# Optimization experiments

Measured on AMD Instinct MI355X. Metric: run time of the kernel, lower is better.

Reference implementation:

```python
import jax, jax.numpy as jnp
import numpy as np

DIM = 1024
H = 16
DH = DIM // H
K = 4
B = 8
N = 2048
EPS = 1e-6


def _depthwise_conv_silu(x, w, n):
    # x: (B, N, C), w: (C, 1, K)  -- torch Conv1d depthwise, padding=K//2, truncate to n, SiLU
    pad = K // 2
    y = jax.lax.conv_general_dilated(
        x.transpose(0, 2, 1), w, window_strides=(1,), padding=[(pad, pad)],
        dimension_numbers=('NCH', 'OIH', 'NCH'), feature_group_count=x.shape[-1])
    y = y[..., :n]  # for even K the conv output is n+1; torch truncates
    return jax.nn.silu(y).transpose(0, 2, 1)


def _l2norm(x):
    return x / (jnp.linalg.norm(x, axis=-1, keepdims=True) + EPS)


def setup_inputs() -> dict:
    key = jax.random.key(0)
    ks = jax.random.split(key, 16)
    s = 1.0 / np.sqrt(DIM)
    d = dict(
        x=jax.random.normal(ks[0], (B, N, DIM), jnp.float32),
        Wq=jax.random.normal(ks[1], (DIM, DIM), jnp.float32) * s,
        bq=jnp.zeros((DIM,), jnp.float32),
        Wk=jax.random.normal(ks[2], (DIM, DIM), jnp.float32) * s,
        bk=jnp.zeros((DIM,), jnp.float32),
        Wv=jax.random.normal(ks[3], (DIM, DIM), jnp.float32) * s,
        bv=jnp.zeros((DIM,), jnp.float32),
        Wa=jax.random.normal(ks[4], (H, DIM), jnp.float32) * s,
        ba=jnp.zeros((H,), jnp.float32),
        Wb=jax.random.normal(ks[5], (H, DIM), jnp.float32) * s,
        bb=jnp.zeros((H,), jnp.float32),
        conv_q=jax.random.normal(ks[6], (DIM, 1, K), jnp.float32) * 0.5,
        conv_k=jax.random.normal(ks[7], (DIM, 1, K), jnp.float32) * 0.5,
        conv_v=jax.random.normal(ks[8], (DIM, 1, K), jnp.float32) * 0.5,
        Wo=jax.random.normal(ks[9], (DIM, DIM), jnp.float32) * s,
        bo=jnp.zeros((DIM,), jnp.float32),
    )
    return d


def _forward(x, Wq, bq, Wk, bk, Wv, bv, Wa, ba, Wb, bb, conv_q, conv_k, conv_v, Wo, bo):
    b_, n_, c_ = x.shape
    q = _l2norm(_depthwise_conv_silu(jax.nn.silu(x @ Wq.T + bq), conv_q, n_))
    k = _l2norm(_depthwise_conv_silu(jax.nn.silu(x @ Wk.T + bk), conv_k, n_))
    v = _depthwise_conv_silu(jax.nn.silu(x @ Wv.T + bv), conv_v, n_)
    a = jax.nn.sigmoid(x @ Wa.T + ba)  # (B, N, H)
    bgate = jax.nn.sigmoid(x @ Wb.T + bb)  # (B, N, H)

    # (N, B, H, Dh) for scan over time
    q = q.reshape(b_, n_, H, DH).transpose(1, 0, 2, 3)
    k = k.reshape(b_, n_, H, DH).transpose(1, 0, 2, 3)
    v = v.reshape(b_, n_, H, DH).transpose(1, 0, 2, 3)
    a = a.transpose(1, 0, 2)
    bgate = bgate.transpose(1, 0, 2)

    S0 = jnp.zeros((b_, H, DH, DH), x.dtype)

    def step(S, inp):
        qt, kt, vt, at, bt = inp  # qt/kt/vt: (B,H,Dh), at/bt: (B,H)
        at = at[..., None, None]
        bt = bt[..., None, None]
        # S_new = S @ (a*(I - b k k^T)) + b * v k^T
        #       = a*S - a*b*(S k) k^T + b * v k^T
        Sk = jnp.einsum('bhde,bhe->bhd', S, kt)
        outer_Sk_k = Sk[..., :, None] * kt[..., None, :]
        outer_v_k = vt[..., :, None] * kt[..., None, :]
        S_new = at * S - at * bt * outer_Sk_k + bt * outer_v_k
        # o_e = sum_d q_d S[d, e]
        ot = jnp.einsum('bhd,bhde->bhe', qt, S_new)
        return S_new, ot

    _, O = jax.lax.scan(step, S0, (q, k, v, a, bgate))  # O: (N, B, H, Dh)
    O = O.transpose(1, 0, 2, 3).reshape(b_, n_, c_)
    return O @ Wo.T + bo


def reference(x, Wq, bq, Wk, bk, Wv, bv, Wa, ba, Wb, bb, conv_q, conv_k, conv_v, Wo, bo):
    return _forward(x, Wq, bq, Wk, bk, Wv, bv, Wa, ba, Wb, bb, conv_q, conv_k, conv_v, Wo, bo)
```

## Files before the change

### kernel.cpp

```cpp
#include <hip/hip_runtime.h>

#define DIMC 1024
#define SEQ  2048
#define NHEAD 16
#define BATCH 8

__device__ __forceinline__ void gll16u(const unsigned short* g, unsigned short* l) {
  __builtin_amdgcn_global_load_lds(
      (const __attribute__((address_space(1))) void*)g,
      (__attribute__((address_space(3))) void*)l, 16, 0, 0);
}
__device__ __forceinline__ void gll16f(const float* g, float* l) {
  __builtin_amdgcn_global_load_lds(
      (const __attribute__((address_space(1))) void*)g,
      (__attribute__((address_space(3))) void*)l, 16, 0, 0);
}

#define WAIT_VM7    0x0F77
#define WAIT_VM0    0x0F70

__device__ __forceinline__ unsigned short f2bf(float f) {
  unsigned u = __float_as_uint(f);
  return (unsigned short)((u + 0x7fffu + ((u >> 16) & 1u)) >> 16);
}
__device__ __forceinline__ float bf2f(unsigned short h) {
  return __uint_as_float(((unsigned)h) << 16);
}

typedef __attribute__((ext_vector_type(8))) short  bf16x8;
typedef __attribute__((ext_vector_type(4))) float  floatx4;

__device__ __forceinline__ float oct_sum(float x) {
  int t1 = __builtin_amdgcn_update_dpp(0, __float_as_int(x), 0xB1, 0xF, 0xF, true);
  float x1 = x + __int_as_float(t1);
  int t2 = __builtin_amdgcn_update_dpp(0, __float_as_int(x1), 0x4E, 0xF, 0xF, true);
  float x2 = x1 + __int_as_float(t2);
  int t3 = __builtin_amdgcn_update_dpp(0, __float_as_int(x2), 0x141, 0xF, 0xF, true);
  return x2 + __int_as_float(t3);
}

__global__ __launch_bounds__(256)
void cvt_split(const float* __restrict__ in, unsigned short* __restrict__ hi,
               unsigned short* __restrict__ lo, int n4)
{
  int i = blockIdx.x * 256 + threadIdx.x;
  if (i >= n4) return;
  float4 f = ((const float4*)in)[i];
  unsigned short h0 = f2bf(f.x), h1 = f2bf(f.y), h2 = f2bf(f.z), h3 = f2bf(f.w);
  unsigned short l0 = f2bf(f.x - bf2f(h0)), l1 = f2bf(f.y - bf2f(h1));
  unsigned short l2 = f2bf(f.z - bf2f(h2)), l3 = f2bf(f.w - bf2f(h3));
  ushort4 H; H.x = h0; H.y = h1; H.z = h2; H.w = h3;
  ushort4 L; L.x = l0; L.y = l1; L.z = l2; L.w = l3;
  ((ushort4*)hi)[i] = H;
  ((ushort4*)lo)[i] = L;
}

__global__ void pack_ab_kernel(const float* __restrict__ Wa, const float* __restrict__ ba,
                               const float* __restrict__ Wb, const float* __restrict__ bb,
                               float* __restrict__ Wab, float* __restrict__ bab)
{
  int i = blockIdx.x * 256 + threadIdx.x;
  if (i < 128 * 1024) {
    int row = i >> 10, col = i & 1023;
    float v = 0.0f;
    if (row < 16) v = Wa[(row << 10) + col];
    else if (row < 32) v = Wb[((row - 16) << 10) + col];
    Wab[i] = v;
  } else {
    int j = i - 128 * 1024;
    if (j < 128) {
      float v = 0.0f;
      if (j < 16) v = ba[j];
      else if (j < 32) v = bb[j - 16];
      bab[j] = v;
    }
  }
}

__global__ __launch_bounds__(256, 2)
void gemm_bf16x3(const unsigned short* __restrict__ Ah, const unsigned short* __restrict__ Al,
                 const unsigned short* __restrict__ Bh, const unsigned short* __restrict__ Bl,
                 const float* __restrict__ bias, float* __restrict__ C,
                 int K, int ldc, int nvalid, int act)
{
  __shared__ unsigned short sAh[4096], sAl[4096], sBh[4096], sBl[4096];
  const int tid  = threadIdx.x;
  const int lane = tid & 63;
  const int w    = tid >> 6;

  const int crow = tid >> 2;
  const int kel  = (tid & 3) << 3;
  const unsigned short* pAh0 = Ah + (size_t)(blockIdx.x * 128 + crow) * K + kel;
  const unsigned short* pAh1 = Ah + (size_t)(blockIdx.x * 128 + 64 + crow) * K + kel;
  const unsigned short* pAl0 = Al + (size_t)(blockIdx.x * 128 + crow) * K + kel;
  const unsigned short* pAl1 = Al + (size_t)(blockIdx.x * 128 + 64 + crow) * K + kel;
  const unsigned short* pBh0 = Bh + (size_t)(blockIdx.y * 128 + crow) * K + kel;
  const unsigned short* pBh1 = Bh + (size_t)(blockIdx.y * 128 + 64 + crow) * K + kel;
  const unsigned short* pBl0 = Bl + (size_t)(blockIdx.y * 128 + crow) * K + kel;
  const unsigned short* pBl1 = Bl + (size_t)(blockIdx.y * 128 + 64 + crow) * K + kel;
  const int wb = (tid & 192) * 8;

  floatx4 acc[16];
  #pragma unroll
  for (int i = 0; i < 16; ++i) acc[i] = (floatx4){0.f, 0.f, 0.f, 0.f};

  const int mq = (w & 1) << 6;
  const int nq = (w >> 1) << 6;
  const int fr = lane & 15;
  const int fk = (lane >> 4) << 3;

  for (int kt = 0; kt < K; kt += 32) {
    __syncthreads();
    gll16u(pAh0, sAh + wb); gll16u(pAh1, sAh + 2048 + wb);
    gll16u(pAl0, sAl + wb); gll16u(pAl1, sAl + 2048 + wb);
    gll16u(pBh0, sBh + wb); gll16u(pBh1, sBh + 2048 + wb);
    gll16u(pBl0, sBl + wb); gll16u(pBl1, sBl + 2048 + wb);
    pAh0 += 32; pAh1 += 32; pAl0 += 32; pAl1 += 32;
    pBh0 += 32; pBh1 += 32; pBl0 += 32; pBl1 += 32;
    __syncthreads();

    bf16x8 ah[4], al[4], bh[4], bl[4];
    #pragma unroll
    for (int mi = 0; mi < 4; ++mi) {
      int off = (mq + mi * 16 + fr) * 32 + fk;
      ah[mi] = *(const bf16x8*)&sAh[off];
      al[mi] = *(const bf16x8*)&sAl[off];
    }
    #pragma unroll
    for (int ni = 0; ni < 4; ++ni) {
      int off = (nq + ni * 16 + fr) * 32 + fk;
      bh[ni] = *(const bf16x8*)&sBh[off];
      bl[ni] = *(const bf16x8*)&sBl[off];
    }
    #pragma unroll
    for (int mi = 0; mi < 4; ++mi)
      #pragma unroll
      for (int ni = 0; ni < 4; ++ni) {
        floatx4 c = acc[mi * 4 + ni];
        c = __builtin_amdgcn_mfma_f32_16x16x32_bf16(ah[mi], bh[ni], c, 0, 0, 0);
        c = __builtin_amdgcn_mfma_f32_16x16x32_bf16(ah[mi], bl[ni], c, 0, 0, 0);
        c = __builtin_amdgcn_mfma_f32_16x16x32_bf16(al[mi], bh[ni], c, 0, 0, 0);
        acc[mi * 4 + ni] = c;
      }
  }

  const int mbase = blockIdx.x * 128 + mq + ((lane >> 4) << 2);
  const int nbase = blockIdx.y * 128 + nq + (lane & 15);
  #pragma unroll
  for (int ni = 0; ni < 4; ++ni) {
    int n = nbase + ni * 16;
    if (n < nvalid) {
      float bs = bias[n];
      #pragma unroll
      for (int mi = 0; mi < 4; ++mi) {
        #pragma unroll
        for (int r = 0; r < 4; ++r) {
          int m = mbase + mi * 16 + r;
          float val = acc[mi * 4 + ni][r] + bs;
          if (act == 1)      val = val * (1.0f / (1.0f + __expf(-val)));
          else if (act == 2) val = 1.0f / (1.0f + __expf(-val));
          C[(size_t)m * ldc + n] = val;
        }
      }
    }
  }
}

__global__ __launch_bounds__(256)
void conv_kernel(const float* __restrict__ pre, const float* __restrict__ w,
                 float* __restrict__ out, int do_norm, int mode)
{
  __shared__ float red[4];
  const int bt  = blockIdx.x;
  const int t   = bt & (SEQ - 1);
  const int tid = threadIdx.x;
  const int c   = tid << 2;
  const float* rowp = pre + (size_t)bt * DIMC + c;
  const float4 z = make_float4(0.f, 0.f, 0.f, 0.f);
  float4 xm2 = (t >= 2)      ? *(const float4*)(rowp - 2 * DIMC) : z;
  float4 xm1 = (t >= 1)      ? *(const float4*)(rowp - DIMC)     : z;
  float4 x0  =                 *(const float4*)(rowp);
  float4 xp1 = (t + 1 < SEQ) ? *(const float4*)(rowp + DIMC)     : z;
  const float4 w0 = *(const float4*)(w + (size_t)(c + 0) * 4);
  const float4 w1 = *(const float4*)(w + (size_t)(c + 1) * 4);
  const float4 w2 = *(const float4*)(w + (size_t)(c + 2) * 4);
  const float4 w3 = *(const float4*)(w + (size_t)(c + 3) * 4);
  float y0 = xm2.x * w0.x + xm1.x * w0.y + x0.x * w0.z + xp1.x * w0.w;
  float y1 = xm2.y * w1.x + xm1.y * w1.y + x0.y * w1.z + xp1.y * w1.w;
  float y2 = xm2.z * w2.x + xm1.z * w2.y + x0.z * w2.z + xp1.z * w2.w;
  float y3 = xm2.w * w3.x + xm1.w * w3.y + x0.w * w3.z + xp1.w * w3.w;
  y0 = y0 * (1.0f / (1.0f + __expf(-y0)));
  y1 = y1 * (1.0f / (1.0f + __expf(-y1)));
  y2 = y2 * (1.0f / (1.0f + __expf(-y2)));
  y3 = y3 * (1.0f / (1.0f + __expf(-y3)));
  if (do_norm) {
    float ss = y0*y0 + y1*y1 + y2*y2 + y3*y3;
    #pragma unroll
    for (int off = 32; off >= 1; off >>= 1) ss += __shfl_xor(ss, off);
    if ((tid & 63) == 0) red[tid >> 6] = ss;
    __syncthreads();
    float tot = red[0] + red[1] + red[2] + red[3];
    float rn = 1.0f / (sqrtf(tot) + 1e-6f);
    y0 *= rn; y1 *= rn; y2 *= rn; y3 *= rn;
  }
  float4 res = make_float4(y0, y1, y2, y3);
  if (mode == 0) {
    *(float4*)(out + (size_t)bt * DIMC + c) = res;
  } else {
    const int b = bt >> 11;
    const int h = c >> 6, e = c & 63;
    const int koff = (mode == 1) ? 0 : 64;
    *(float4*)(out + (((size_t)(b * 16 + h)) * SEQ + t) * 128 + koff + e) = res;
  }
}

#define PD 16
__global__ __launch_bounds__(64)
void scan2_kernel(const float* __restrict__ kv, const float* __restrict__ ab,
                  float* __restrict__ Cf, float* __restrict__ SC)
{
  __shared__ float ring[8][256];
  __shared__ float aS[SEQ];
  __shared__ float bSh[SEQ];
  __shared__ float cbuf[8][72];
  const int bh  = blockIdx.x;
  const int dg  = blockIdx.y;
  const int b   = bh >> 4, h = bh & 15;
  const int tid = threadIdx.x;
  const int eh  = tid & 7;
  const int dl  = tid >> 3;
  const int d   = dg * 8 + dl;
  const int e0  = eh * 8;

  const float* abbase = ab + (size_t)b * SEQ * 32 + h;
  for (int i = tid; i < SEQ; i += 64) {
    aS[i]  = abbase[(size_t)i * 32];
    bSh[i] = abbase[(size_t)i * 32 + 16];
  }

  const float* kvsrc = kv + (size_t)bh * SEQ * 128 + tid * 4;

  {
    float4 z4 = make_float4(0.f, 0.f, 0.f, 0.f);
    float4* dst0 = (float4*)&SC[(((size_t)bh * 32) * 64 + d) * 64 + e0];
    dst0[0] = z4; dst0[1] = z4;
  }

  #pragma unroll
  for (int pp = 0; pp < 8; ++pp)
    gll16f(kvsrc + (size_t)pp * 256, &ring[pp][0]);
  __builtin_amdgcn_s_waitcnt(WAIT_VM0);
  asm volatile("" ::: "memory");

  float S[8];
  #pragma unroll
  for (int j = 0; j < 8; ++j) S[j] = 0.f;

  float4 k1a = *(const float4*)&ring[0][e0];
  float4 k1b = *(const float4*)&ring[0][e0 + 4];
  float  v1  = ring[0][64 + d];
  float4 k2a = *(const float4*)&ring[0][128 + e0];
  float4 k2b = *(const float4*)&ring[0][128 + e0 + 4];
  float  v2  = ring[0][192 + d];
  float  a1  = aS[0], a2 = aS[1];
  float  b1  = bSh[0], b2 = bSh[1];

  for (int t = 0; t < SEQ; t += 2) {
    float q0 = fmaf(S[0], k1a.x, S[4] * k1b.x);
    float q1 = fmaf(S[1], k1a.y, S[5] * k1b.y);
    float q2 = fmaf(S[2], k1a.z, S[6] * k1b.z);
    float q3 = fmaf(S[3], k1a.w, S[7] * k1b.w);
    float r0 = fmaf(S[0], k2a.x, S[4] * k2b.x);
    float r1 = fmaf(S[1], k2a.y, S[5] * k2b.y);
    float r2 = fmaf(S[2], k2a.z, S[6] * k2b.z);
    float r3 = fmaf(S[3], k2a.w, S[7] * k2b.w);
    float x0 = fmaf(k1a.x, k2a.x, k1b.x * k2b.x);
    float x1 = fmaf(k1a.y, k2a.y, k1b.y * k2b.y);
    float x2 = fmaf(k1a.z, k2a.z, k1b.z * k2b.z);
    float x3 = fmaf(k1a.w, k2a.w, k1b.w * k2b.w);
    float u1  = oct_sum((q0 + q1) + (q2 + q3));
    float u2  = oct_sum((r0 + r1) + (r2 + r3));
    float kap = oct_sum((x0 + x1) + (x2 + x3));

    const float e1c = b1 * v1, f1 = a1 * b1;
    const float e2c = b2 * v2, f2 = a2 * b2;
    const float w2c = a1 * u2;
    const float G2  = a1 * a2;
    const float c1  = fmaf(-f1, u1, e1c);
    const float c2  = fmaf(-f2, fmaf(c1, kap, w2c), e2c);
    const float d1  = a2 * c1;
    if (eh == 0) {
      float2* cw = (float2*)&cbuf[dl][t & 63];
      *cw = make_float2(c1, c2);
    }

    asm volatile("" ::: "memory");
    if (t < SEQ - PD) {
      const int slot = (t >> 1) & 7;
      gll16f(kvsrc + (size_t)(t + PD) * 128, &ring[slot][0]);
      asm volatile("" ::: "memory");
      __builtin_amdgcn_s_waitcnt(WAIT_VM7);
    } else {
      asm volatile("" ::: "memory");
      __builtin_amdgcn_s_waitcnt(WAIT_VM0);
    }
    asm volatile("" ::: "memory");

    const int sl = ((t >> 1) + 1) & 7;
    const int tn = (t + 2) & (SEQ - 1);
    const float4 k1a_n = *(const float4*)&ring[sl][e0];
    const float4 k1b_n = *(const float4*)&ring[sl][e0 + 4];
    const float  v1_n  = ring[sl][64 + d];
    const float4 k2a_n = *(const float4*)&ring[sl][128 + e0];
    const float4 k2b_n = *(const float4*)&ring[sl][128 + e0 + 4];
    const float  v2_n  = ring[sl][192 + d];
    const float2 a_n   = *(const float2*)&aS[tn];
    const float2 b_n   = *(const float2*)&bSh[tn];

    S[0] = fmaf(G2, S[0], fmaf(d1, k1a.x, c2 * k2a.x));
    S[1] = fmaf(G2, S[1], fmaf(d1, k1a.y, c2 * k2a.y));
    S[2] = fmaf(G2, S[2], fmaf(d1, k1a.z, c2 * k2a.z));
    S[3] = fmaf(G2, S[3], fmaf(d1, k1a.w, c2 * k2a.w));
    S[4] = fmaf(G2, S[4], fmaf(d1, k1b.x, c2 * k2b.x));
    S[5] = fmaf(G2, S[5], fmaf(d1, k1b.y, c2 * k2b.y));
    S[6] = fmaf(G2, S[6], fmaf(d1, k1b.z, c2 * k2b.z));
    S[7] = fmaf(G2, S[7], fmaf(d1, k1b.w, c2 * k2b.w));

    if (((t + 2) & 63) == 0) {
      const int cix  = t >> 6;
      const int d2l  = tid >> 3;
      const int toff = (tid & 7) << 3;
      float* dst = Cf + (((size_t)bh * 32 + cix) * 64 + dg * 8 + d2l) * 64 + toff;
      float4 f0 = *(const float4*)&cbuf[d2l][toff];
      float4 f1 = *(const float4*)&cbuf[d2l][toff + 4];
      *(float4*)dst       = f0;
      *(float4*)(dst + 4) = f1;
      if ((t + 2) < SEQ) {
        float4* ck = (float4*)&SC[(((size_t)bh * 32 + ((t + 2) >> 6)) * 64 + d) * 64 + e0];
        ck[0] = make_float4(S[0], S[1], S[2], S[3]);
        ck[1] = make_float4(S[4], S[5], S[6], S[7]);
      }
    }

    k1a = k1a_n; k1b = k1b_n; k2a = k2a_n; k2b = k2b_n;
    v1 = v1_n; v2 = v2_n; a1 = a_n.x; a2 = a_n.y; b1 = b_n.x; b2 = b_n.y;
  }
}

__global__ __launch_bounds__(256)
void outp_kernel(const float* __restrict__ q, const float* __restrict__ kv,
                 const float* __restrict__ Cf, const float* __restrict__ SC,
                 const float* __restrict__ ab, float* __restrict__ O)
{
  __shared__ float QsT[64 * 64];
  __shared__ float CP [64 * 64];
  __shared__ float Ks [64 * 64];
  __shared__ float Zs [64 * 64];
  __shared__ float av[64], Gv[64], rGv[64];

  const int c   = blockIdx.x;
  const int bh  = blockIdx.y;
  const int b   = bh >> 4, h = bh & 15;
  const int cs  = c << 6;
  const int tid = threadIdx.x;
  const int tl  = tid & 63, th = tid >> 6;

  {
    const float* qr = q + ((size_t)(b * SEQ + cs + tl)) * DIMC + h * 64 + th * 16;
    #pragma unroll
    for (int u = 0; u < 4; ++u) {
      float4 qv = *(const float4*)(qr + u * 4);
      int dd = th * 16 + u * 4;
      QsT[(dd+0)*64 + tl] = qv.x; QsT[(dd+1)*64 + tl] = qv.y;
      QsT[(dd+2)*64 + tl] = qv.z; QsT[(dd+3)*64 + tl] = qv.w;
    }
    const float* cr = Cf + ((size_t)bh * 32 + c) * 4096;
    #pragma unroll
    for (int u = 0; u < 4; ++u)
      *(float4*)&CP[tid * 16 + u * 4] = *(const float4*)(cr + tid * 16 + u * 4);
    const float* kr = kv + ((size_t)bh * SEQ + cs + tl) * 128 + th * 16;
    const float* zr = SC + (((size_t)bh * 32 + c) * 64 + tl) * 64 + th * 16;
    #pragma unroll
    for (int u = 0; u < 4; ++u) {
      *(float4*)&Ks[tl * 64 + th * 16 + u * 4] = *(const float4*)(kr + u * 4);
      *(float4*)&Zs[tl * 64 + th * 16 + u * 4] = *(const float4*)(zr + u * 4);
    }
    if (tid < 64) av[tid] = ab[((size_t)(b * SEQ + cs + tid)) * 32 + h];
  }
  __syncthreads();
  if (tid == 0) {
    float g = 1.f;
    for (int t = 0; t < 64; ++t) { g *= av[t]; Gv[t] = fmaxf(g, 1e-37f); }
  }
  __syncthreads();
  if (tid < 64) rGv[tid] = 1.0f / Gv[tid];
  __syncthreads();

  const int tq = (tid >> 4) << 2;
  const int s0 = (tid & 15) << 2;

  float p[4][4] = {{0.f}};
  #pragma unroll 4
  for (int dd = 0; dd < 64; ++dd) {
    const float4 qv = *(const float4*)&QsT[dd * 64 + tq];
    const float4 cv = *(const float4*)&CP [dd * 64 + s0];
    const float qa[4] = {qv.x, qv.y, qv.z, qv.w};
    const float ca[4] = {cv.x, cv.y, cv.z, cv.w};
    #pragma unroll
    for (int i = 0; i < 4; ++i)
      #pragma unroll
      for (int j = 0; j < 4; ++j)
        p[i][j] = fmaf(qa[i], ca[j], p[i][j]);
  }
  __syncthreads();

  #pragma unroll
  for (int i = 0; i < 4; ++i) {
    const float gt = Gv[tq + i];
    #pragma unroll
    for (int j = 0; j < 4; ++j) {
      float vsc = (s0 + j <= tq + i) ? p[i][j] * gt * rGv[s0 + j] : 0.f;
      CP[(s0 + j) * 64 + (tq + i)] = vsc;
    }
  }
  __syncthreads();

  const int e0 = s0;
  float o[4][4] = {{0.f}};
  #pragma unroll 4
  for (int ss = 0; ss < 64; ++ss) {
    const float4 pv = *(const float4*)&CP[ss * 64 + tq];
    const float4 kvv = *(const float4*)&Ks[ss * 64 + e0];
    const float pa[4] = {pv.x, pv.y, pv.z, pv.w};
    const float ka[4] = {kvv.x, kvv.y, kvv.z, kvv.w};
    #pragma unroll
    for (int i = 0; i < 4; ++i)
      #pragma unroll
      for (int j = 0; j < 4; ++j)
        o[i][j] = fmaf(pa[i], ka[j], o[i][j]);
  }
  float zt[4][4] = {{0.f}};
  #pragma unroll 4
  for (int dd = 0; dd < 64; ++dd) {
    const float4 qv = *(const float4*)&QsT[dd * 64 + tq];
    const float4 zv = *(const float4*)&Zs[dd * 64 + e0];
    const float qa[4] = {qv.x, qv.y, qv.z, qv.w};
    const float za[4] = {zv.x, zv.y, zv.z, zv.w};
    #pragma unroll
    for (int i = 0; i < 4; ++i)
      #pragma unroll
      for (int j = 0; j < 4; ++j)
        zt[i][j] = fmaf(qa[i], za[j], zt[i][j]);
  }
  #pragma unroll
  for (int i = 0; i < 4; ++i) {
    const float gt = Gv[tq + i];
    float4 res;
    res.x = fmaf(gt, zt[i][0], o[i][0]);
    res.y = fmaf(gt, zt[i][1], o[i][1]);
    res.z = fmaf(gt, zt[i][2], o[i][2]);
    res.w = fmaf(gt, zt[i][3], o[i][3]);
    *(float4*)(O + ((size_t)(b * SEQ + cs + tq + i)) * DIMC + h * 64 + e0) = res;
  }
}

extern "C" void kernel_launch(void* const* d_in, const int* in_sizes, int n_in,
                              void* d_out, int out_size, void* d_ws, size_t ws_size,
                              hipStream_t stream)
{
  const float* x  = (const float*)d_in[0];
  const float* Wq = (const float*)d_in[1];
  const float* bq = (const float*)d_in[2];
  const float* Wk = (const float*)d_in[3];
  const float* bk = (const float*)d_in[4];
  const float* Wv = (const float*)d_in[5];
  const float* bv = (const float*)d_in[6];
  const float* Wa = (const float*)d_in[7];
  const float* ba = (const float*)d_in[8];
  const float* Wb = (const float*)d_in[9];
  const float* bb = (const float*)d_in[10];
  const float* cq = (const float*)d_in[11];
  const float* ck = (const float*)d_in[12];
  const float* cv = (const float*)d_in[13];
  const float* Wo = (const float*)d_in[14];
  const float* bo = (const float*)d_in[15];
  float* out = (float*)d_out;
  float* ws  = (float*)d_ws;

  const size_t per_b = (size_t)SEQ * DIMC;
  const size_t wsz   = (size_t)DIMC * DIMC;

  int bc = BATCH;
  while (bc > 1) {
    size_t fl = 4 * (size_t)bc * per_b + (size_t)bc * SEQ * 32 + 128 * 1024 + 128;
    size_t us = 2 * (size_t)bc * per_b + 8 * wsz + 2 * 128 * 1024;
    if (fl * 4 + us * 2 <= ws_size) break;
    bc >>= 1;
  }

  float* P   = ws;
  float* qb  = P  + (size_t)bc * per_b;
  float* kvp = qb + (size_t)bc * per_b;
  float* abb = kvp + 2 * (size_t)bc * per_b;
  float* Wab = abb + (size_t)bc * SEQ * 32;
  float* bab = Wab + 128 * 1024;
  unsigned short* xh   = (unsigned short*)(bab + 128);
  unsigned short* xl   = xh  + (size_t)bc * per_b;
  unsigned short* wqh  = xl  + (size_t)bc * per_b;
  unsigned short* wql  = wqh + wsz;
  unsigned short* wkh  = wql + wsz;
  unsigned short* wkl  = wkh + wsz;
  unsigned short* wvh  = wkl + wsz;
  unsigned short* wvl  = wvh + wsz;
  unsigned short* woh  = wvl + wsz;
  unsigned short* wol  = woh + wsz;
  unsigned short* wabh = wol + wsz;
  unsigned short* wabl = wabh + 128 * 1024;

  float* Cf  = (float*)xh;
  float* SCp = P;

  pack_ab_kernel<<<513, 256, 0, stream>>>(Wa, ba, Wb, bb, Wab, bab);
  cvt_split<<<(int)(wsz / 4 + 255) / 256, 256, 0, stream>>>(Wq, wqh, wql, (int)(wsz / 4));
  cvt_split<<<(int)(wsz / 4 + 255) / 256, 256, 0, stream>>>(Wk, wkh, wkl, (int)(wsz / 4));
  cvt_split<<<(int)(wsz / 4 + 255) / 256, 256, 0, stream>>>(Wv, wvh, wvl, (int)(wsz / 4));
  cvt_split<<<(int)(wsz / 4 + 255) / 256, 256, 0, stream>>>(Wo, woh, wol, (int)(wsz / 4));
  cvt_split<<<(128 * 1024 / 4 + 255) / 256, 256, 0, stream>>>(Wab, wabh, wabl, 128 * 1024 / 4);

  for (int b0 = 0; b0 < BATCH; b0 += bc) {
    const float* xb = x + (size_t)b0 * per_b;
    float* outb = out + (size_t)b0 * per_b;
    const int M = bc * SEQ;
    const int n4 = (int)((size_t)bc * per_b / 4);
    const int nbh = bc * NHEAD;
    dim3 gg(M / 128, DIMC / 128);
    dim3 gab(M / 128, 1);

    cvt_split<<<(n4 + 255) / 256, 256, 0, stream>>>(xb, xh, xl, n4);

    gemm_bf16x3<<<gg, 256, 0, stream>>>(xh, xl, wqh, wql, bq, P, DIMC, DIMC, DIMC, 1);
    conv_kernel<<<dim3(M), 256, 0, stream>>>(P, cq, qb, 1, 0);
    gemm_bf16x3<<<gg, 256, 0, stream>>>(xh, xl, wkh, wkl, bk, P, DIMC, DIMC, DIMC, 1);
    conv_kernel<<<dim3(M), 256, 0, stream>>>(P, ck, kvp, 1, 1);
    gemm_bf16x3<<<gg, 256, 0, stream>>>(xh, xl, wvh, wvl, bv, P, DIMC, DIMC, DIMC, 1);
    conv_kernel<<<dim3(M), 256, 0, stream>>>(P, cv, kvp, 0, 2);
    gemm_bf16x3<<<gab, 256, 0, stream>>>(xh, xl, wabh, wabl, bab, abb, DIMC, 32, 32, 2);
    scan2_kernel<<<dim3(nbh, 8), 64, 0, stream>>>(kvp, abb, Cf, SCp);
    outp_kernel<<<dim3(SEQ / 64, nbh), 256, 0, stream>>>(qb, kvp, Cf, SCp, abb, outb);
    cvt_split<<<(n4 + 255) / 256, 256, 0, stream>>>(outb, xh, xl, n4);
    gemm_bf16x3<<<gg, 256, 0, stream>>>(xh, xl, woh, wol, bo, outb, DIMC, DIMC, DIMC, 0);
  }
}
```

Baseline: 1.562 ms.

## Process four recurrence steps per iteration in the delta-rule state scan

The sequential scan now advances the state by four timesteps per iteration instead of two. It computes the pairwise key dot products and the chained coefficients c1..c4, then applies a single fused rank-4 update to S. This halves the number of serial loop iterations and their cross-lane reductions and syncs per timestep. In exchange it needs more reductions per iteration (10 instead of 3), more registers, two prefetches per iteration and a changed wait count, and it reassociates the floating-point arithmetic.

New measurement: 1.586 ms. About the same (+1.6%).

```diff
diff --git a/kernel.cpp b/kernel.cpp
--- a/kernel.cpp
+++ b/kernel.cpp
@@ -16,7 +16,7 @@
       (__attribute__((address_space(3))) void*)l, 16, 0, 0);
 }
 
-#define WAIT_VM7    0x0F77
+#define WAIT_VM6    0x0F76
 #define WAIT_VM0    0x0F70
 
 __device__ __forceinline__ unsigned short f2bf(float f) {
@@ -262,88 +262,131 @@
   float4 k2a = *(const float4*)&ring[0][128 + e0];
   float4 k2b = *(const float4*)&ring[0][128 + e0 + 4];
   float  v2  = ring[0][192 + d];
-  float  a1  = aS[0], a2 = aS[1];
-  float  b1  = bSh[0], b2 = bSh[1];
-
-  for (int t = 0; t < SEQ; t += 2) {
-    float q0 = fmaf(S[0], k1a.x, S[4] * k1b.x);
-    float q1 = fmaf(S[1], k1a.y, S[5] * k1b.y);
-    float q2 = fmaf(S[2], k1a.z, S[6] * k1b.z);
-    float q3 = fmaf(S[3], k1a.w, S[7] * k1b.w);
-    float r0 = fmaf(S[0], k2a.x, S[4] * k2b.x);
-    float r1 = fmaf(S[1], k2a.y, S[5] * k2b.y);
-    float r2 = fmaf(S[2], k2a.z, S[6] * k2b.z);
-    float r3 = fmaf(S[3], k2a.w, S[7] * k2b.w);
-    float x0 = fmaf(k1a.x, k2a.x, k1b.x * k2b.x);
-    float x1 = fmaf(k1a.y, k2a.y, k1b.y * k2b.y);
-    float x2 = fmaf(k1a.z, k2a.z, k1b.z * k2b.z);
-    float x3 = fmaf(k1a.w, k2a.w, k1b.w * k2b.w);
-    float u1  = oct_sum((q0 + q1) + (q2 + q3));
-    float u2  = oct_sum((r0 + r1) + (r2 + r3));
-    float kap = oct_sum((x0 + x1) + (x2 + x3));
-
-    const float e1c = b1 * v1, f1 = a1 * b1;
-    const float e2c = b2 * v2, f2 = a2 * b2;
-    const float w2c = a1 * u2;
-    const float G2  = a1 * a2;
-    const float c1  = fmaf(-f1, u1, e1c);
-    const float c2  = fmaf(-f2, fmaf(c1, kap, w2c), e2c);
-    const float d1  = a2 * c1;
-    if (eh == 0) {
-      float2* cw = (float2*)&cbuf[dl][t & 63];
-      *cw = make_float2(c1, c2);
-    }
+  float4 k3a = *(const float4*)&ring[1][e0];
+  float4 k3b = *(const float4*)&ring[1][e0 + 4];
+  float  v3  = ring[1][64 + d];
+  float4 k4a = *(const float4*)&ring[1][128 + e0];
+  float4 k4b = *(const float4*)&ring[1][128 + e0 + 4];
+  float  v4  = ring[1][192 + d];
+  float4 av  = *(const float4*)&aS[0];
+  float4 bv  = *(const float4*)&bSh[0];
+
+  for (int t = 0; t < SEQ; t += 4) {
+    const float a1 = av.x, a2 = av.y, a3 = av.z, a4 = av.w;
+    const float b1 = bv.x, b2 = bv.y, b3 = bv.z, b4 = bv.w;
+
+    float p0, p1, p2, p3;
+    p0 = fmaf(S[0], k1a.x, S[4] * k1b.x); p1 = fmaf(S[1], k1a.y, S[5] * k1b.y);
+    p2 = fmaf(S[2], k1a.z, S[6] * k1b.z); p3 = fmaf(S[3], k1a.w, S[7] * k1b.w);
+    float u1 = oct_sum((p0 + p1) + (p2 + p3));
+    p0 = fmaf(S[0], k2a.x, S[4] * k2b.x); p1 = fmaf(S[1], k2a.y, S[5] * k2b.y);
+    p2 = fmaf(S[2], k2a.z, S[6] * k2b.z); p3 = fmaf(S[3], k2a.w, S[7] * k2b.w);
+    float u2 = oct_sum((p0 + p1) + (p2 + p3));
+    p0 = fmaf(S[0], k3a.x, S[4] * k3b.x); p1 = fmaf(S[1], k3a.y, S[5] * k3b.y);
+    p2 = fmaf(S[2], k3a.z, S[6] * k3b.z); p3 = fmaf(S[3], k3a.w, S[7] * k3b.w);
+    float u3 = oct_sum((p0 + p1) + (p2 + p3));
+    p0 = fmaf(S[0], k4a.x, S[4] * k4b.x); p1 = fmaf(S[1], k4a.y, S[5] * k4b.y);
+    p2 = fmaf(S[2], k4a.z, S[6] * k4b.z); p3 = fmaf(S[3], k4a.w, S[7] * k4b.w);
+    float u4 = oct_sum((p0 + p1) + (p2 + p3));
+    p0 = fmaf(k1a.x, k2a.x, k1b.x * k2b.x); p1 = fmaf(k1a.y, k2a.y, k1b.y * k2b.y);
+    p2 = fmaf(k1a.z, k2a.z, k1b.z * k2b.z); p3 = fmaf(k1a.w, k2a.w, k1b.w * k2b.w);
+    float K12 = oct_sum((p0 + p1) + (p2 + p3));
+    p0 = fmaf(k1a.x, k3a.x, k1b.x * k3b.x); p1 = fmaf(k1a.y, k3a.y, k1b.y * k3b.y);
+    p2 = fmaf(k1a.z, k3a.z, k1b.z * k3b.z); p3 = fmaf(k1a.w, k3a.w, k1b.w * k3b.w);
+    float K13 = oct_sum((p0 + p1) + (p2 + p3));
+    p0 = fmaf(k2a.x, k3a.x, k2b.x * k3b.x); p1 = fmaf(k2a.y, k3a.y, k2b.y * k3b.y);
+    p2 = fmaf(k2a.z, k3a.z, k2b.z * k3b.z); p3 = fmaf(k2a.w, k3a.w, k2b.w * k3b.w);
+    float K23 = oct_sum((p0 + p1) + (p2 + p3));
+    p0 = fmaf(k1a.x, k4a.x, k1b.x * k4b.x); p1 = fmaf(k1a.y, k4a.y, k1b.y * k4b.y);
+    p2 = fmaf(k1a.z, k4a.z, k1b.z * k4b.z); p3 = fmaf(k1a.w, k4a.w, k1b.w * k4b.w);
+    float K14 = oct_sum((p0 + p1) + (p2 + p3));
+    p0 = fmaf(k2a.x, k4a.x, k2b.x * k4b.x); p1 = fmaf(k2a.y, k4a.y, k2b.y * k4b.y);
+    p2 = fmaf(k2a.z, k4a.z, k2b.z * k4b.z); p3 = fmaf(k2a.w, k4a.w, k2b.w * k4b.w);
+    float K24 = oct_sum((p0 + p1) + (p2 + p3));
+    p0 = fmaf(k3a.x, k4a.x, k3b.x * k4b.x); p1 = fmaf(k3a.y, k4a.y, k3b.y * k4b.y);
+    p2 = fmaf(k3a.z, k4a.z, k3b.z * k4b.z); p3 = fmaf(k3a.w, k4a.w, k3b.w * k4b.w);
+    float K34 = oct_sum((p0 + p1) + (p2 + p3));
+
+    const float f1 = a1 * b1, f2 = a2 * b2, f3 = a3 * b3, f4 = a4 * b4;
+    const float e1 = b1 * v1, e2 = b2 * v2, e3 = b3 * v3, e4 = b4 * v4;
+    const float a1u2 = a1 * u2, a1u3 = a1 * u3, a1u4 = a1 * u4;
+    const float a34 = a3 * a4, a234 = a2 * a34, G = a1 * a234;
+    const float c1 = fmaf(-f1, u1, e1);
+    const float c2 = fmaf(-f2, fmaf(c1, K12, a1u2), e2);
+    const float m3 = fmaf(a2, fmaf(c1, K13, a1u3), c2 * K23);
+    const float c3 = fmaf(-f3, m3, e3);
+    const float m4 = fmaf(a3, fmaf(a2, fmaf(c1, K14, a1u4), c2 * K24), c3 * K34);
+    const float c4 = fmaf(-f4, m4, e4);
+    const float d1 = c1 * a234, d2 = c2 * a34, d3 = c3 * a4;
+
+    if (eh == 0)
+      *(float4*)&cbuf[dl][t & 63] = make_float4(c1, c2, c3, c4);
 
     asm volatile("" ::: "memory");
     if (t < SEQ - PD) {
-      const int slot = (t >> 1) & 7;
-      gll16f(kvsrc + (size_t)(t + PD) * 128, &ring[slot][0]);
+      const int p = t >> 1;
+      gll16f(kvsrc + (size_t)(t + PD) * 128,     &ring[p & 7][0]);
+      gll16f(kvsrc + (size_t)(t + PD + 2) * 128, &ring[(p + 1) & 7][0]);
       asm volatile("" ::: "memory");
-      __builtin_amdgcn_s_waitcnt(WAIT_VM7);
+      __builtin_amdgcn_s_waitcnt(WAIT_VM6);
     } else {
       asm volatile("" ::: "memory");
       __builtin_amdgcn_s_waitcnt(WAIT_VM0);
     }
     asm volatile("" ::: "memory");
 
-    const int sl = ((t >> 1) + 1) & 7;
-    const int tn = (t + 2) & (SEQ - 1);
-    const float4 k1a_n = *(const float4*)&ring[sl][e0];
-    const float4 k1b_n = *(const float4*)&ring[sl][e0 + 4];
-    const float  v1_n  = ring[sl][64 + d];
-    const float4 k2a_n = *(const float4*)&ring[sl][128 + e0];
-    const float4 k2b_n = *(const float4*)&ring[sl][128 + e0 + 4];
-    const float  v2_n  = ring[sl][192 + d];
-    const float2 a_n   = *(const float2*)&aS[tn];
-    const float2 b_n   = *(const float2*)&bSh[tn];
-
-    S[0] = fmaf(G2, S[0], fmaf(d1, k1a.x, c2 * k2a.x));
-    S[1] = fmaf(G2, S[1], fmaf(d1, k1a.y, c2 * k2a.y));
-    S[2] = fmaf(G2, S[2], fmaf(d1, k1a.z, c2 * k2a.z));
-    S[3] = fmaf(G2, S[3], fmaf(d1, k1a.w, c2 * k2a.w));
-    S[4] = fmaf(G2, S[4], fmaf(d1, k1b.x, c2 * k2b.x));
-    S[5] = fmaf(G2, S[5], fmaf(d1, k1b.y, c2 * k2b.y));
-    S[6] = fmaf(G2, S[6], fmaf(d1, k1b.z, c2 * k2b.z));
-    S[7] = fmaf(G2, S[7], fmaf(d1, k1b.w, c2 * k2b.w));
-
-    if (((t + 2) & 63) == 0) {
+    #pragma unroll
+    for (int j = 0; j < 4; ++j) {
+      const float* K1 = &k1a.x; const float* K2 = &k2a.x;
+      const float* K3 = &k3a.x; const float* K4 = &k4a.x;
+      float t1 = fmaf(d1, K1[j], d2 * K2[j]);
+      float t2 = fmaf(d3, K3[j], c4 * K4[j]);
+      S[j] = fmaf(G, S[j], t1 + t2);
+    }
+    #pragma unroll
+    for (int j = 0; j < 4; ++j) {
+      const float* K1 = &k1b.x; const float* K2 = &k2b.x;
+      const float* K3 = &k3b.x; const float* K4 = &k4b.x;
+      float t1 = fmaf(d1, K1[j], d2 * K2[j]);
+      float t2 = fmaf(d3, K3[j], c4 * K4[j]);
+      S[4 + j] = fmaf(G, S[4 + j], t1 + t2);
+    }
+
+    {
+      const int sl2 = ((t >> 1) + 2) & 7;
+      const int sl3 = ((t >> 1) + 3) & 7;
+      const int tn  = (t + 4) & (SEQ - 1);
+      k1a = *(const float4*)&ring[sl2][e0];
+      k1b = *(const float4*)&ring[sl2][e0 + 4];
+      v1  = ring[sl2][64 + d];
+      k2a = *(const float4*)&ring[sl2][128 + e0];
+      k2b = *(const float4*)&ring[sl2][128 + e0 + 4];
+      v2  = ring[sl2][192 + d];
+      k3a = *(const float4*)&ring[sl3][e0];
+      k3b = *(const float4*)&ring[sl3][e0 + 4];
+      v3  = ring[sl3][64 + d];
+      k4a = *(const float4*)&ring[sl3][128 + e0];
+      k4b = *(const float4*)&ring[sl3][128 + e0 + 4];
+      v4  = ring[sl3][192 + d];
+      av  = *(const float4*)&aS[tn];
+      bv  = *(const float4*)&bSh[tn];
+    }
+
+    if (((t + 4) & 63) == 0) {
       const int cix  = t >> 6;
       const int d2l  = tid >> 3;
       const int toff = (tid & 7) << 3;
       float* dst = Cf + (((size_t)bh * 32 + cix) * 64 + dg * 8 + d2l) * 64 + toff;
-      float4 f0 = *(const float4*)&cbuf[d2l][toff];
-      float4 f1 = *(const float4*)&cbuf[d2l][toff + 4];
-      *(float4*)dst       = f0;
-      *(float4*)(dst + 4) = f1;
-      if ((t + 2) < SEQ) {
-        float4* ck = (float4*)&SC[(((size_t)bh * 32 + ((t + 2) >> 6)) * 64 + d) * 64 + e0];
+      float4 f0v = *(const float4*)&cbuf[d2l][toff];
+      float4 f1v = *(const float4*)&cbuf[d2l][toff + 4];
+      *(float4*)dst       = f0v;
+      *(float4*)(dst + 4) = f1v;
+      if ((t + 4) < SEQ) {
+        float4* ck = (float4*)&SC[(((size_t)bh * 32 + ((t + 4) >> 6)) * 64 + d) * 64 + e0];
         ck[0] = make_float4(S[0], S[1], S[2], S[3]);
         ck[1] = make_float4(S[4], S[5], S[6], S[7]);
       }
     }
-
-    k1a = k1a_n; k1b = k1b_n; k2a = k2a_n; k2b = k2b_n;
-    v1 = v1_n; v2 = v2_n; a1 = a_n.x; a2 = a_n.y; b1 = b_n.x; b2 = b_n.y;
   }
 }
 
```
